# Kernel tuning notes

Hardware: AMD Instinct MI355X
Metric: run time of the kernel (lower is better)

## Reference

```python
import jax, jax.numpy as jnp
import numpy as np

NEG_SLOPE = 0.2


def gat_conv(x, W, att_s, att_d, bias, src, dst, heads, out_c, concat):
    n = x.shape[0]
    h = (x @ W).reshape(n, heads, out_c)                      # [N,H,C]
    a_s = (h * att_s).sum(-1)                                 # [N,H]
    a_d = (h * att_d).sum(-1)                                 # [N,H]
    logits = jax.nn.leaky_relu(a_s[src] + a_d[dst], NEG_SLOPE)  # [E,H]
    # segment softmax over incoming edges of each dst node (per head)
    m = jax.ops.segment_max(logits, dst, num_segments=n)
    e = jnp.exp(logits - m[dst])
    denom = jax.ops.segment_sum(e, dst, num_segments=n)
    alpha = e / denom[dst]                                    # [E,H]
    msg = h[src] * alpha[:, :, None]                          # [E,H,C]
    out = jax.ops.segment_sum(msg, dst, num_segments=n)       # [N,H,C]
    out = out.reshape(n, heads * out_c) if concat else out.mean(axis=1)
    return out + bias


def setup_inputs() -> dict:
    key = jax.random.key(0)
    ks = jax.random.split(key, 9)
    N, IN, OUT, E = 100000, 256, 40, 1600000
    return {
        "x": jax.random.normal(ks[0], (N, IN), jnp.float32),
        "edge_index": jax.random.randint(ks[1], (2, E), 0, N, jnp.int32),
        "W1": jax.random.normal(ks[2], (IN, 64), jnp.float32) * (1.0 / np.sqrt(IN)),
        "att_src1": jax.random.normal(ks[3], (8, 8), jnp.float32) * 0.1,
        "att_dst1": jax.random.normal(ks[4], (8, 8), jnp.float32) * 0.1,
        "b1": jnp.zeros((64,), jnp.float32),
        "W2": jax.random.normal(ks[5], (64, OUT), jnp.float32) * (1.0 / 8.0),
        "att_src2": jax.random.normal(ks[6], (1, OUT), jnp.float32) * 0.1,
        "att_dst2": jax.random.normal(ks[7], (1, OUT), jnp.float32) * 0.1,
        "b2": jnp.zeros((OUT,), jnp.float32),
    }


def reference(x, edge_index, W1, att_src1, att_dst1, b1, W2, att_src2, att_dst2, b2):
    n = x.shape[0]
    loop = jnp.arange(n, dtype=edge_index.dtype)
    src = jnp.concatenate([edge_index[0], loop])  # self-loops (PyG default)
    dst = jnp.concatenate([edge_index[1], loop])
    h = gat_conv(x, W1, att_src1, att_dst1, b1, src, dst, heads=8, out_c=8, concat=True)
    h = jax.nn.relu(h)
    out = gat_conv(h, W2, att_src2, att_dst2, b2, src, dst, heads=1, out_c=W2.shape[1], concat=True)
    return jax.nn.log_softmax(out, axis=1)
```

## Files before the change

### kernel.cpp

```cpp
#include <hip/hip_runtime.h>


#define L_IN   256
#define L_C1   64
#define L_H1   8
#define L_OUT  40
#define BCAP   5120

typedef __attribute__((ext_vector_type(8))) short short8;
typedef __attribute__((ext_vector_type(4))) float f32x4;

__device__ __forceinline__ float leaky(float x){ return fmaxf(x, 0.2f*x); }
__device__ __forceinline__ unsigned f2bf(float f){
  unsigned u = __float_as_uint(f);
  return (u + 0x7fffu + ((u >> 16) & 1u)) >> 16;
}
__device__ __forceinline__ float bflo(unsigned u){ return __uint_as_float(u << 16); }
__device__ __forceinline__ float bfhi(unsigned u){ return __uint_as_float(u & 0xffff0000u); }


__global__ __launch_bounds__(256) void bin_scatter(const int* __restrict__ esrc,
    const int* __restrict__ edst, int* __restrict__ gcur,
    unsigned* __restrict__ binned, int E, int NB){
  __shared__ int hist[512], rbase[512], cur[512];
  const int t  = threadIdx.x;
  const int e0 = blockIdx.x * 4096;
  hist[t] = 0; hist[t+256] = 0; cur[t] = 0; cur[t+256] = 0;
  __syncthreads();
  int sv[16], dv[16];
  const bool full = (e0 + 4096 <= E);
  if (full){
    #pragma unroll
    for (int j = 0; j < 4; ++j){
      int p4 = (e0 >> 2) + j*256 + t;
      int4 s4 = ((const int4*)esrc)[p4];
      int4 d4 = ((const int4*)edst)[p4];
      sv[4*j+0]=s4.x; sv[4*j+1]=s4.y; sv[4*j+2]=s4.z; sv[4*j+3]=s4.w;
      dv[4*j+0]=d4.x; dv[4*j+1]=d4.y; dv[4*j+2]=d4.z; dv[4*j+3]=d4.w;
      atomicAdd(&hist[d4.x >> 8], 1); atomicAdd(&hist[d4.y >> 8], 1);
      atomicAdd(&hist[d4.z >> 8], 1); atomicAdd(&hist[d4.w >> 8], 1);
    }
  } else {
    #pragma unroll
    for (int j = 0; j < 16; ++j){
      int idx = e0 + j*256 + t;
      if (idx < E){
        sv[j] = esrc[idx]; dv[j] = edst[idx];
        atomicAdd(&hist[dv[j] >> 8], 1);
      } else dv[j] = -1;
    }
  }
  __syncthreads();
  if (hist[t])                   rbase[t]     = atomicAdd(&gcur[t],     hist[t]);
  if (t+256 < NB && hist[t+256]) rbase[t+256] = atomicAdd(&gcur[t+256], hist[t+256]);
  __syncthreads();
  #pragma unroll
  for (int j = 0; j < 16; ++j){
    if (dv[j] >= 0){
      int b = dv[j] >> 8;
      int off = rbase[b] + atomicAdd(&cur[b], 1);
      if (off < BCAP)
        binned[(size_t)b*BCAP + off] =
          (unsigned)sv[j] | ((unsigned)(dv[j] & 255) << 17);
    }
  }
}

__global__ __launch_bounds__(256) void bucket_csr(const unsigned* __restrict__ binned,
    const int* __restrict__ gcur, int2* __restrict__ nodeptr, int* __restrict__ csr,
    int N){
  __shared__ unsigned ebuf[BCAP];
  __shared__ int cnt[256], pref[256], cur[256];
  const int t = threadIdx.x;
  const int b = blockIdx.x;
  int ne = gcur[b]; if (ne > BCAP) ne = BCAP;
  const int base = b * BCAP;
  cnt[t] = 0; cur[t] = 0;
  __syncthreads();
  for (int i = t; i < ne; i += 256){
    unsigned e = binned[base + i];
    ebuf[i] = e;
    atomicAdd(&cnt[(e >> 17) & 255u], 1);
  }
  __syncthreads();
  pref[t] = cnt[t];
  __syncthreads();
  for (int off = 1; off < 256; off <<= 1){
    int a = (t >= off) ? pref[t-off] : 0;
    __syncthreads();
    pref[t] += a;
    __syncthreads();
  }
  int excl = pref[t] - cnt[t];
  __syncthreads();
  pref[t] = excl;
  int d = (b << 8) + t;
  if (d < N) nodeptr[d] = make_int2(base + excl, cnt[t]);
  __syncthreads();
  for (int i = t; i < ne; i += 256){
    unsigned e = ebuf[i];
    int ln = (int)((e >> 17) & 255u);
    int pos = base + pref[ln] + atomicAdd(&cur[ln], 1);
    csr[pos] = (int)(e & 0x1FFFFu);
  }
}

__global__ __launch_bounds__(256) void prep_w1(const float* __restrict__ W1,
                                               ushort* __restrict__ wt){
  __shared__ float ws[64][65];
  const int t  = threadIdx.x;
  const int kb = blockIdx.x;
  #pragma unroll
  for (int i = 0; i < 16; ++i){
    int idx = t + i*256;
    ws[idx >> 6][idx & 63] = W1[(size_t)(kb*64 + (idx >> 6))*64 + (idx & 63)];
  }
  __syncthreads();
  int c  = t >> 2;
  int j0 = (t & 3) * 16;
  ushort tmp[16];
  #pragma unroll
  for (int j = 0; j < 16; ++j) tmp[j] = (ushort)f2bf(ws[j0 + j][c]);
  uint4* dst = (uint4*)(wt + (size_t)c*256 + kb*64 + j0);
  dst[0] = *(uint4*)&tmp[0];
  dst[1] = *(uint4*)&tmp[8];
}

__global__ __launch_bounds__(256) void gemm1_kernel(
    const float* __restrict__ x, const ushort* __restrict__ wt,
    const float* __restrict__ atts, const float* __restrict__ attd,
    ushort* __restrict__ h1b, float* __restrict__ as1, float* __restrict__ ad1, int n)
{
  __shared__ ushort xs[64][136];
  __shared__ ushort ws[64][136];
  __shared__ ushort hs[64][72];
  const int t  = threadIdx.x;
  const int rb = blockIdx.x * 64;
  const int wv = t >> 6;
  const int ln = t & 63;
  const int fr = ln & 15;
  const int fq = ln >> 4;

  f32x4 acc[4];
  #pragma unroll
  for (int cb = 0; cb < 4; ++cb) acc[cb] = (f32x4){0.f,0.f,0.f,0.f};

  for (int kb = 0; kb < 2; ++kb){
    if (kb) __syncthreads();
    #pragma unroll
    for (int i = 0; i < 8; ++i){
      int idx = t + i*256;
      int row = idx >> 5, c4 = idx & 31;
      float4 v = make_float4(0.f,0.f,0.f,0.f);
      if (rb + row < n) v = *(const float4*)(x + (size_t)(rb+row)*L_IN + kb*128 + c4*4);
      uint2 p;
      p.x = f2bf(v.x) | (f2bf(v.y) << 16);
      p.y = f2bf(v.z) | (f2bf(v.w) << 16);
      *(uint2*)&xs[row][c4*4] = p;
    }
    #pragma unroll
    for (int i = 0; i < 4; ++i){
      int idx = t + i*256;
      int row = idx >> 4, c8 = idx & 15;
      *(uint4*)&ws[row][c8*8] = *(const uint4*)(wt + (size_t)row*256 + kb*128 + c8*8);
    }
    __syncthreads();
    #pragma unroll
    for (int ks = 0; ks < 4; ++ks){
      short8 a = *(const short8*)&xs[wv*16 + fr][ks*32 + fq*8];
      #pragma unroll
      for (int cb = 0; cb < 4; ++cb){
        short8 b = *(const short8*)&ws[cb*16 + fr][ks*32 + fq*8];
        acc[cb] = __builtin_amdgcn_mfma_f32_16x16x32_bf16(a, b, acc[cb], 0, 0, 0);
      }
    }
  }
  __syncthreads();
  #pragma unroll
  for (int cb = 0; cb < 4; ++cb)
    #pragma unroll
    for (int r = 0; r < 4; ++r)
      hs[wv*16 + fq*4 + r][cb*16 + fr] = (ushort)f2bf(acc[cb][r]);
  __syncthreads();
  #pragma unroll
  for (int p = 0; p < 2; ++p){
    int pid = t + p*256;
    int row = pid >> 3, hd = pid & 7;
    if (rb + row < n){
      uint4 u = *(const uint4*)&hs[row][hd*8];
      float v0=bflo(u.x), v1=bfhi(u.x), v2=bflo(u.y), v3=bfhi(u.y);
      float v4=bflo(u.z), v5=bfhi(u.z), v6=bflo(u.w), v7=bfhi(u.w);
      const float* sa = atts + hd*8;
      const float* da = attd + hd*8;
      float ds = v0*sa[0]+v1*sa[1]+v2*sa[2]+v3*sa[3]+v4*sa[4]+v5*sa[5]+v6*sa[6]+v7*sa[7];
      float dd = v0*da[0]+v1*da[1]+v2*da[2]+v3*da[3]+v4*da[4]+v5*da[5]+v6*da[6]+v7*da[7];
      as1[(size_t)(rb+row)*L_H1 + hd] = ds;
      ad1[(size_t)(rb+row)*L_H1 + hd] = dd;
    }
  }
  #pragma unroll
  for (int i = 0; i < 2; ++i){
    int idx = t + i*256;
    int row = idx >> 3, c8 = idx & 7;
    if (rb + row < n)
      *(uint4*)(h1b + (size_t)(rb+row)*L_C1 + c8*8) = *(const uint4*)&hs[row][c8*8];
  }
}

__global__ __launch_bounds__(256) void agg1_kernel(
    const int2* __restrict__ nodeptr, const int* __restrict__ csr,
    const ushort* __restrict__ h1b, const float* __restrict__ as1,
    const float* __restrict__ ad1, const float* __restrict__ b1,
    ushort* __restrict__ hrb, int n)
{
  int wid  = (blockIdx.x*blockDim.x + threadIdx.x) >> 6;
  int lane = threadIdx.x & 63;
  if (wid >= n) return;
  int2 np  = nodeptr[wid];
  int beg  = np.x;
  int degt = np.y + 1;

  const int h  = lane & 7;
  const int eg = lane >> 3;
  const int cp = lane & 31;
  const int ep = lane >> 5;
  const int hc = cp >> 2;

  float adn = ad1[(size_t)wid*L_H1 + h];
  float ax = 0.f, ay = 0.f, sp = 0.f;

  #define A1_GRP_W(g, SRCV, WV)                                            \
    { int i_ = (g)*8 + eg;                                                 \
      SRCV = (i_ < degt-1) ? csr[beg + i_] : wid;                          \
      float l_ = (i_ < degt) ? leaky(as1[(size_t)SRCV*L_H1 + h] + adn)     \
                             : -1e30f;                                     \
      WV = __expf(l_); sp += WV; }
  #define A1_GRP_G(SRCV, WV)                                               \
    _Pragma("unroll")                                                      \
    for (int e0 = 0; e0 < 8; e0 += 2){                                     \
      int e_  = e0 + ep;                                                   \
      float we_ = __shfl(WV,   e_*8 + hc);                                 \
      int   se_ = __shfl(SRCV, e_*8);                                      \
      unsigned u_ = *(const unsigned*)(h1b + (size_t)se_*L_C1 + cp*2);     \
      ax += we_ * bflo(u_);                                                \
      ay += we_ * bfhi(u_);                                                \
    }

  if (degt <= 16){
    int s0, s1; float w0, w1;
    A1_GRP_W(0, s0, w0) A1_GRP_W(1, s1, w1)
    A1_GRP_G(s0, w0) A1_GRP_G(s1, w1)
  } else if (degt <= 24){
    int s0, s1, s2; float w0, w1, w2;
    A1_GRP_W(0, s0, w0) A1_GRP_W(1, s1, w1) A1_GRP_W(2, s2, w2)
    A1_GRP_G(s0, w0) A1_GRP_G(s1, w1) A1_GRP_G(s2, w2)
  } else {
    const int ngrp = (degt + 7) >> 3;
    for (int g = 0; g < ngrp; ++g){
      int sg; float wg;
      A1_GRP_W(g, sg, wg)
      A1_GRP_G(sg, wg)
    }
  }
  #undef A1_GRP_W
  #undef A1_GRP_G

  #pragma unroll
  for (int off = 8; off < 64; off <<= 1) sp += __shfl_xor(sp, off);
  float rinv = 1.0f / __shfl(sp, hc);
  ax += __shfl_xor(ax, 32);
  ay += __shfl_xor(ay, 32);
  if (lane < 32){
    float2 bv = *(const float2*)&b1[cp*2];
    float r0 = fmaxf(ax*rinv + bv.x, 0.f);
    float r1 = fmaxf(ay*rinv + bv.y, 0.f);
    *(unsigned*)(hrb + (size_t)wid*L_C1 + cp*2) = f2bf(r0) | (f2bf(r1) << 16);
  }
}

__global__ __launch_bounds__(256) void gemm2_kernel(
    const ushort* __restrict__ hrb, const float* __restrict__ W2,
    const float* __restrict__ atts2, const float* __restrict__ attd2,
    ushort* __restrict__ h2b, float* __restrict__ as2, float* __restrict__ ad2, int n)
{
  __shared__ float w2s[64*40];
  const int t = threadIdx.x;
  for (int i = t; i < 64*40; i += 256) w2s[i] = W2[i];
  __syncthreads();
  int row = blockIdx.x*256 + t;
  if (row >= n) return;

  uint4 rv[8];
  #pragma unroll
  for (int q = 0; q < 8; ++q)
    rv[q] = *(const uint4*)(hrb + (size_t)row*L_C1 + q*8);

  f32x4 acc4[10];
  #pragma unroll
  for (int j = 0; j < 10; ++j) acc4[j] = (f32x4){0.f,0.f,0.f,0.f};

  #pragma unroll
  for (int q = 0; q < 8; ++q){
    unsigned uu[4] = {rv[q].x, rv[q].y, rv[q].z, rv[q].w};
    #pragma unroll
    for (int d = 0; d < 4; ++d){
      int k = q*8 + d*2;
      float v0 = bflo(uu[d]), v1 = bfhi(uu[d]);
      const f32x4* w0 = (const f32x4*)&w2s[k*40];
      const f32x4* w1 = (const f32x4*)&w2s[(k+1)*40];
      #pragma unroll
      for (int j = 0; j < 10; ++j) acc4[j] += v0*w0[j] + v1*w1[j];
    }
  }

  float acc[40];
  #pragma unroll
  for (int j = 0; j < 10; ++j){
    acc[4*j+0]=acc4[j][0]; acc[4*j+1]=acc4[j][1];
    acc[4*j+2]=acc4[j][2]; acc[4*j+3]=acc4[j][3];
  }
  float ps = 0.f, pd = 0.f;
  #pragma unroll
  for (int j = 0; j < 40; ++j){ ps += acc[j]*atts2[j]; pd += acc[j]*attd2[j]; }
  unsigned pk[20];
  #pragma unroll
  for (int q = 0; q < 20; ++q) pk[q] = f2bf(acc[2*q]) | (f2bf(acc[2*q+1]) << 16);
  uint4* dst = (uint4*)(h2b + (size_t)row*L_OUT);
  #pragma unroll
  for (int q = 0; q < 5; ++q) dst[q] = make_uint4(pk[4*q],pk[4*q+1],pk[4*q+2],pk[4*q+3]);
  as2[row] = ps;
  ad2[row] = pd;
}

__global__ __launch_bounds__(256) void agg2_kernel(
    const int2* __restrict__ nodeptr, const int* __restrict__ csr,
    const ushort* __restrict__ h2b, const float* __restrict__ as2,
    const float* __restrict__ ad2, const float* __restrict__ b2,
    float* __restrict__ out, int n)
{
  int wid  = (blockIdx.x*blockDim.x + threadIdx.x) >> 6;
  int lane = threadIdx.x & 63;
  if (wid >= n) return;
  int2 np  = nodeptr[wid];
  int beg  = np.x;
  int degt = np.y + 1;

  const int eidx = (lane < 60) ? (lane / 20) : 0;
  const int cq   = (lane < 60) ? (lane % 20) : 0;

  float adn = ad2[wid];
  float ax = 0.f, ay = 0.f, sp = 0.f;

  #define A2_STEP(e_, SRCV, WV, CNT)                                       \
    { int ee_ = (e_);                                                      \
      int es_ = (ee_ < 64) ? ee_ : 63;                                     \
      float we_ = __shfl(WV,   es_);                                       \
      int   se_ = __shfl(SRCV, es_);                                       \
      we_ = (ee_ < (CNT)) ? we_ : 0.f;                                     \
      unsigned u_ = *(const unsigned*)(h2b + (size_t)se_*L_OUT + cq*2);    \
      ax += we_ * bflo(u_);                                                \
      ay += we_ * bfhi(u_); }

  if (degt <= 64){
    int i = lane;
    int src = (i < degt-1) ? csr[beg + i] : wid;
    float l = (i < degt) ? leaky(as2[src] + adn) : -1e30f;
    float w = __expf(l);
    sp = w;
    if (degt <= 18){
      #pragma unroll
      for (int j = 0; j < 2; ++j){
        A2_STEP(j*9 + 0*3 + eidx, src, w, degt)
        A2_STEP(j*9 + 1*3 + eidx, src, w, degt)
        A2_STEP(j*9 + 2*3 + eidx, src, w, degt)
      }
    } else if (degt <= 27){
      #pragma unroll
      for (int j = 0; j < 3; ++j){
        A2_STEP(j*9 + 0*3 + eidx, src, w, degt)
        A2_STEP(j*9 + 1*3 + eidx, src, w, degt)
        A2_STEP(j*9 + 2*3 + eidx, src, w, degt)
      }
    } else if (degt <= 36){
      #pragma unroll
      for (int j = 0; j < 4; ++j){
        A2_STEP(j*9 + 0*3 + eidx, src, w, degt)
        A2_STEP(j*9 + 1*3 + eidx, src, w, degt)
        A2_STEP(j*9 + 2*3 + eidx, src, w, degt)
      }
    } else {
      for (int e0 = 0; e0 < degt; e0 += 9){
        A2_STEP(e0 + 0*3 + eidx, src, w, degt)
        A2_STEP(e0 + 1*3 + eidx, src, w, degt)
        A2_STEP(e0 + 2*3 + eidx, src, w, degt)
      }
    }
  } else {
    const int ngrp = (degt + 63) >> 6;
    for (int g = 0; g < ngrp; ++g){
      int i = g*64 + lane;
      int src = (i < degt-1) ? csr[beg + i] : wid;
      float l = (i < degt) ? leaky(as2[src] + adn) : -1e30f;
      float w = __expf(l);
      sp += w;
      int cnt = degt - g*64; if (cnt > 64) cnt = 64;
      for (int e0 = 0; e0 < cnt; e0 += 9){
        A2_STEP(e0 + 0*3 + eidx, src, w, cnt)
        A2_STEP(e0 + 1*3 + eidx, src, w, cnt)
        A2_STEP(e0 + 2*3 + eidx, src, w, cnt)
      }
    }
  }
  #undef A2_STEP

  #pragma unroll
  for (int off = 1; off < 64; off <<= 1) sp += __shfl_xor(sp, off);
  float rinv = 1.0f / sp;

  float ax0 = __shfl(ax, cq), ax1 = __shfl(ax, cq+20), ax2 = __shfl(ax, cq+40);
  float ay0 = __shfl(ay, cq), ay1 = __shfl(ay, cq+20), ay2 = __shfl(ay, cq+40);
  float axs = (ax0 + ax1) + ax2;
  float ays = (ay0 + ay1) + ay2;

  bool act = (lane < 20);
  float o0 = axs*rinv + b2[cq*2];
  float o1 = ays*rinv + b2[cq*2+1];
  float mx = act ? fmaxf(o0, o1) : -1e30f;
  #pragma unroll
  for (int off = 1; off < 32; off <<= 1) mx = fmaxf(mx, __shfl_xor(mx, off));
  float ex = act ? (__expf(o0 - mx) + __expf(o1 - mx)) : 0.f;
  #pragma unroll
  for (int off = 1; off < 32; off <<= 1) ex += __shfl_xor(ex, off);
  float lse = mx + __logf(ex);
  if (act){
    float2 r = make_float2(o0 - lse, o1 - lse);
    *(float2*)(out + (size_t)wid*L_OUT + cq*2) = r;
  }
}

extern "C" void kernel_launch(void* const* d_in, const int* in_sizes, int n_in,
                              void* d_out, int out_size, void* d_ws, size_t ws_size,
                              hipStream_t stream)
{
  const float* x    = (const float*)d_in[0];
  const int*   ei   = (const int*)  d_in[1];
  const float* W1   = (const float*)d_in[2];
  const float* as1w = (const float*)d_in[3];
  const float* ad1w = (const float*)d_in[4];
  const float* b1   = (const float*)d_in[5];
  const float* W2   = (const float*)d_in[6];
  const float* as2w = (const float*)d_in[7];
  const float* ad2w = (const float*)d_in[8];
  const float* b2   = (const float*)d_in[9];

  const int N = in_sizes[0] / L_IN;
  const int E = in_sizes[1] / 2;
  const int NB = (N + 255) >> 8;
  const int* esrc = ei;
  const int* edst = ei + E;
  float* out = (float*)d_out;

  char* w = (char*)d_ws;
  auto alloc = [&](size_t bytes)->char*{
    char* p = w; w += (bytes + 255) & ~size_t(255); return p;
  };
  ushort* h1b  = (ushort*)alloc((size_t)N*L_C1*2);
  float*  as1  = (float*) alloc((size_t)N*L_H1*4);
  float*  ad1  = (float*) alloc((size_t)N*L_H1*4);
  size_t union_sz = (size_t)N*L_C1*2 + (size_t)N*L_OUT*2;
  if (union_sz < (size_t)NB*BCAP*4) union_sz = (size_t)NB*BCAP*4;
  char*  ub    = alloc(union_sz);
  ushort* hrb  = (ushort*)ub;
  ushort* h2b  = (ushort*)(ub + (size_t)N*L_C1*2);
  unsigned* binned = (unsigned*)ub;
  float*  as2  = (float*) alloc((size_t)N*4);
  float*  ad2  = (float*) alloc((size_t)N*4);
  ushort* wt   = (ushort*)alloc((size_t)64*256*2);
  int2*  nodeptr=(int2*)  alloc((size_t)N*8);
  int*   csr   = (int*)   alloc((size_t)NB*BCAP*4);
  int*   gcur  = (int*)   alloc((size_t)NB*4);

  hipMemsetAsync(gcur, 0, (size_t)NB*4, stream);

  prep_w1    <<<4,              256, 0, stream>>>(W1, wt);
  bin_scatter<<<(E+4095)/4096,  256, 0, stream>>>(esrc, edst, gcur, binned, E, NB);
  bucket_csr <<<NB,             256, 0, stream>>>(binned, gcur, nodeptr, csr, N);

  gemm1_kernel<<<(N+63)/64,     256, 0, stream>>>(x, wt, as1w, ad1w, h1b, as1, ad1, N);
  agg1_kernel <<<(N+3)/4,       256, 0, stream>>>(nodeptr, csr, h1b, as1, ad1, b1, hrb, N);
  gemm2_kernel<<<(N+255)/256,   256, 0, stream>>>(hrb, W2, as2w, ad2w, h2b, as2, ad2, N);
  agg2_kernel <<<(N+3)/4,       256, 0, stream>>>(nodeptr, csr, h2b, as2, ad2, b2, out, N);
}
```

Before: 192.1 us.

## Merge edge binning with GEMM1 in one launch and fold memset into prep

Edge binning (bin_scatter) and the first dense GEMM become a single kernel, with blocks split by index: the first NSC blocks bin edges and the rest compute GEMM1 rows. The two independent workloads can then run concurrently, and one launch is removed. Zeroing of the gcur counters moves from hipMemsetAsync into an extra block of prep_w1, removing another launch. The combined kernel takes the larger shared-memory footprint, which may reduce occupancy for the scatter blocks.

```diff
diff --git a/kernel.cpp b/kernel.cpp
--- a/kernel.cpp
+++ b/kernel.cpp
@@ -18,97 +18,15 @@
 __device__ __forceinline__ float bflo(unsigned u){ return __uint_as_float(u << 16); }
 __device__ __forceinline__ float bfhi(unsigned u){ return __uint_as_float(u & 0xffff0000u); }
 
-
-__global__ __launch_bounds__(256) void bin_scatter(const int* __restrict__ esrc,
-    const int* __restrict__ edst, int* __restrict__ gcur,
-    unsigned* __restrict__ binned, int E, int NB){
-  __shared__ int hist[512], rbase[512], cur[512];
-  const int t  = threadIdx.x;
-  const int e0 = blockIdx.x * 4096;
-  hist[t] = 0; hist[t+256] = 0; cur[t] = 0; cur[t+256] = 0;
-  __syncthreads();
-  int sv[16], dv[16];
-  const bool full = (e0 + 4096 <= E);
-  if (full){
-    #pragma unroll
-    for (int j = 0; j < 4; ++j){
-      int p4 = (e0 >> 2) + j*256 + t;
-      int4 s4 = ((const int4*)esrc)[p4];
-      int4 d4 = ((const int4*)edst)[p4];
-      sv[4*j+0]=s4.x; sv[4*j+1]=s4.y; sv[4*j+2]=s4.z; sv[4*j+3]=s4.w;
-      dv[4*j+0]=d4.x; dv[4*j+1]=d4.y; dv[4*j+2]=d4.z; dv[4*j+3]=d4.w;
-      atomicAdd(&hist[d4.x >> 8], 1); atomicAdd(&hist[d4.y >> 8], 1);
-      atomicAdd(&hist[d4.z >> 8], 1); atomicAdd(&hist[d4.w >> 8], 1);
-    }
-  } else {
-    #pragma unroll
-    for (int j = 0; j < 16; ++j){
-      int idx = e0 + j*256 + t;
-      if (idx < E){
-        sv[j] = esrc[idx]; dv[j] = edst[idx];
-        atomicAdd(&hist[dv[j] >> 8], 1);
-      } else dv[j] = -1;
-    }
-  }
-  __syncthreads();
-  if (hist[t])                   rbase[t]     = atomicAdd(&gcur[t],     hist[t]);
-  if (t+256 < NB && hist[t+256]) rbase[t+256] = atomicAdd(&gcur[t+256], hist[t+256]);
-  __syncthreads();
-  #pragma unroll
-  for (int j = 0; j < 16; ++j){
-    if (dv[j] >= 0){
-      int b = dv[j] >> 8;
-      int off = rbase[b] + atomicAdd(&cur[b], 1);
-      if (off < BCAP)
-        binned[(size_t)b*BCAP + off] =
-          (unsigned)sv[j] | ((unsigned)(dv[j] & 255) << 17);
-    }
-  }
-}
-
-__global__ __launch_bounds__(256) void bucket_csr(const unsigned* __restrict__ binned,
-    const int* __restrict__ gcur, int2* __restrict__ nodeptr, int* __restrict__ csr,
-    int N){
-  __shared__ unsigned ebuf[BCAP];
-  __shared__ int cnt[256], pref[256], cur[256];
+__global__ __launch_bounds__(256) void prep_w1(const float* __restrict__ W1,
+                                               ushort* __restrict__ wt,
+                                               int* __restrict__ gcur, int NB){
   const int t = threadIdx.x;
-  const int b = blockIdx.x;
-  int ne = gcur[b]; if (ne > BCAP) ne = BCAP;
-  const int base = b * BCAP;
-  cnt[t] = 0; cur[t] = 0;
-  __syncthreads();
-  for (int i = t; i < ne; i += 256){
-    unsigned e = binned[base + i];
-    ebuf[i] = e;
-    atomicAdd(&cnt[(e >> 17) & 255u], 1);
-  }
-  __syncthreads();
-  pref[t] = cnt[t];
-  __syncthreads();
-  for (int off = 1; off < 256; off <<= 1){
-    int a = (t >= off) ? pref[t-off] : 0;
-    __syncthreads();
-    pref[t] += a;
-    __syncthreads();
-  }
-  int excl = pref[t] - cnt[t];
-  __syncthreads();
-  pref[t] = excl;
-  int d = (b << 8) + t;
-  if (d < N) nodeptr[d] = make_int2(base + excl, cnt[t]);
-  __syncthreads();
-  for (int i = t; i < ne; i += 256){
-    unsigned e = ebuf[i];
-    int ln = (int)((e >> 17) & 255u);
-    int pos = base + pref[ln] + atomicAdd(&cur[ln], 1);
-    csr[pos] = (int)(e & 0x1FFFFu);
-  }
-}
-
-__global__ __launch_bounds__(256) void prep_w1(const float* __restrict__ W1,
-                                               ushort* __restrict__ wt){
+  if (blockIdx.x == 4){
+    for (int i = t; i < NB; i += 256) gcur[i] = 0;
+    return;
+  }
   __shared__ float ws[64][65];
-  const int t  = threadIdx.x;
   const int kb = blockIdx.x;
   #pragma unroll
   for (int i = 0; i < 16; ++i){
@@ -126,16 +44,67 @@
   dst[1] = *(uint4*)&tmp[8];
 }
 
-__global__ __launch_bounds__(256) void gemm1_kernel(
+__global__ __launch_bounds__(256) void scatter_gemm1(
+    const int* __restrict__ esrc, const int* __restrict__ edst,
+    int* __restrict__ gcur, unsigned* __restrict__ binned, int E, int NB, int NSC,
     const float* __restrict__ x, const ushort* __restrict__ wt,
     const float* __restrict__ atts, const float* __restrict__ attd,
     ushort* __restrict__ h1b, float* __restrict__ as1, float* __restrict__ ad1, int n)
 {
-  __shared__ ushort xs[64][136];
-  __shared__ ushort ws[64][136];
-  __shared__ ushort hs[64][72];
-  const int t  = threadIdx.x;
-  const int rb = blockIdx.x * 64;
+  __shared__ __align__(16) char smem[44032];
+  const int t = threadIdx.x;
+
+  if ((int)blockIdx.x < NSC){
+    int* hist  = (int*)smem;
+    int* rbase = hist + 512;
+    int* cur   = rbase + 512;
+    const int e0 = blockIdx.x * 4096;
+    hist[t] = 0; hist[t+256] = 0; cur[t] = 0; cur[t+256] = 0;
+    __syncthreads();
+    int sv[16], dv[16];
+    const bool full = (e0 + 4096 <= E);
+    if (full){
+      #pragma unroll
+      for (int j = 0; j < 4; ++j){
+        int p4 = (e0 >> 2) + j*256 + t;
+        int4 s4 = ((const int4*)esrc)[p4];
+        int4 d4 = ((const int4*)edst)[p4];
+        sv[4*j+0]=s4.x; sv[4*j+1]=s4.y; sv[4*j+2]=s4.z; sv[4*j+3]=s4.w;
+        dv[4*j+0]=d4.x; dv[4*j+1]=d4.y; dv[4*j+2]=d4.z; dv[4*j+3]=d4.w;
+        atomicAdd(&hist[d4.x >> 8], 1); atomicAdd(&hist[d4.y >> 8], 1);
+        atomicAdd(&hist[d4.z >> 8], 1); atomicAdd(&hist[d4.w >> 8], 1);
+      }
+    } else {
+      #pragma unroll
+      for (int j = 0; j < 16; ++j){
+        int idx = e0 + j*256 + t;
+        if (idx < E){
+          sv[j] = esrc[idx]; dv[j] = edst[idx];
+          atomicAdd(&hist[dv[j] >> 8], 1);
+        } else dv[j] = -1;
+      }
+    }
+    __syncthreads();
+    if (hist[t])                   rbase[t]     = atomicAdd(&gcur[t],     hist[t]);
+    if (t+256 < NB && hist[t+256]) rbase[t+256] = atomicAdd(&gcur[t+256], hist[t+256]);
+    __syncthreads();
+    #pragma unroll
+    for (int j = 0; j < 16; ++j){
+      if (dv[j] >= 0){
+        int b = dv[j] >> 8;
+        int off = rbase[b] + atomicAdd(&cur[b], 1);
+        if (off < BCAP)
+          binned[(size_t)b*BCAP + off] =
+            (unsigned)sv[j] | ((unsigned)(dv[j] & 255) << 17);
+      }
+    }
+    return;
+  }
+
+  ushort (*xs)[136] = (ushort(*)[136])(smem);
+  ushort (*ws)[136] = (ushort(*)[136])(smem + 17408);
+  ushort (*hs)[72]  = (ushort(*)[72]) (smem + 34816);
+  const int rb = (blockIdx.x - NSC) * 64;
   const int wv = t >> 6;
   const int ln = t & 63;
   const int fr = ln & 15;
@@ -204,6 +173,45 @@
     int row = idx >> 3, c8 = idx & 7;
     if (rb + row < n)
       *(uint4*)(h1b + (size_t)(rb+row)*L_C1 + c8*8) = *(const uint4*)&hs[row][c8*8];
+  }
+}
+
+__global__ __launch_bounds__(256) void bucket_csr(const unsigned* __restrict__ binned,
+    const int* __restrict__ gcur, int2* __restrict__ nodeptr, int* __restrict__ csr,
+    int N){
+  __shared__ unsigned ebuf[BCAP];
+  __shared__ int cnt[256], pref[256], cur[256];
+  const int t = threadIdx.x;
+  const int b = blockIdx.x;
+  int ne = gcur[b]; if (ne > BCAP) ne = BCAP;
+  const int base = b * BCAP;
+  cnt[t] = 0; cur[t] = 0;
+  __syncthreads();
+  for (int i = t; i < ne; i += 256){
+    unsigned e = binned[base + i];
+    ebuf[i] = e;
+    atomicAdd(&cnt[(e >> 17) & 255u], 1);
+  }
+  __syncthreads();
+  pref[t] = cnt[t];
+  __syncthreads();
+  for (int off = 1; off < 256; off <<= 1){
+    int a = (t >= off) ? pref[t-off] : 0;
+    __syncthreads();
+    pref[t] += a;
+    __syncthreads();
+  }
+  int excl = pref[t] - cnt[t];
+  __syncthreads();
+  pref[t] = excl;
+  int d = (b << 8) + t;
+  if (d < N) nodeptr[d] = make_int2(base + excl, cnt[t]);
+  __syncthreads();
+  for (int i = t; i < ne; i += 256){
+    unsigned e = ebuf[i];
+    int ln = (int)((e >> 17) & 255u);
+    int pos = base + pref[ln] + atomicAdd(&cur[ln], 1);
+    csr[pos] = (int)(e & 0x1FFFFu);
   }
 }
 
@@ -456,6 +464,8 @@
   const int N = in_sizes[0] / L_IN;
   const int E = in_sizes[1] / 2;
   const int NB = (N + 255) >> 8;
+  const int NSC = (E + 4095) / 4096;
+  const int NG1 = (N + 63) / 64;
   const int* esrc = ei;
   const int* edst = ei + E;
   float* out = (float*)d_out;
@@ -480,14 +490,11 @@
   int*   csr   = (int*)   alloc((size_t)NB*BCAP*4);
   int*   gcur  = (int*)   alloc((size_t)NB*4);
 
-  hipMemsetAsync(gcur, 0, (size_t)NB*4, stream);
-
-  prep_w1    <<<4,              256, 0, stream>>>(W1, wt);
-  bin_scatter<<<(E+4095)/4096,  256, 0, stream>>>(esrc, edst, gcur, binned, E, NB);
-  bucket_csr <<<NB,             256, 0, stream>>>(binned, gcur, nodeptr, csr, N);
-
-  gemm1_kernel<<<(N+63)/64,     256, 0, stream>>>(x, wt, as1w, ad1w, h1b, as1, ad1, N);
-  agg1_kernel <<<(N+3)/4,       256, 0, stream>>>(nodeptr, csr, h1b, as1, ad1, b1, hrb, N);
-  gemm2_kernel<<<(N+255)/256,   256, 0, stream>>>(hrb, W2, as2w, ad2w, h2b, as2, ad2, N);
-  agg2_kernel <<<(N+3)/4,       256, 0, stream>>>(nodeptr, csr, h2b, as2, ad2, b2, out, N);
-}
+  prep_w1     <<<5,          256, 0, stream>>>(W1, wt, gcur, NB);
+  scatter_gemm1<<<NSC + NG1, 256, 0, stream>>>(esrc, edst, gcur, binned, E, NB, NSC,
+                                               x, wt, as1w, ad1w, h1b, as1, ad1, N);
+  bucket_csr  <<<NB,         256, 0, stream>>>(binned, gcur, nodeptr, csr, N);
+  agg1_kernel <<<(N+3)/4,    256, 0, stream>>>(nodeptr, csr, h1b, as1, ad1, b1, hrb, N);
+  gemm2_kernel<<<(N+255)/256,256, 0, stream>>>(hrb, W2, as2w, ad2w, h2b, as2, ad2, N);
+  agg2_kernel <<<(N+3)/4,    256, 0, stream>>>(nodeptr, csr, h2b, as2, ad2, b2, out, N);
+}
```

New measurement: 180.2 us. -6.2%, faster.
